# Kernel tuning notes

Measured on AMD Instinct MI355X. Metric: run time of the kernel, lower is better.

Reference implementation:

```python
import jax, jax.numpy as jnp
import numpy as np

B, N, M, H = 32, 1024, 256, 128


def setup_inputs() -> dict:
    key = jax.random.key(0)
    kA, kh, kW1, kW2 = jax.random.split(key, 4)
    A = jax.random.uniform(kA, (B, N, N), dtype=jnp.float32)
    h = jax.random.normal(kh, (B, N, M), dtype=jnp.float32)
    # torch Linear default init scale ~ 1/sqrt(fan_in)
    W1 = jax.random.normal(kW1, (M, H), dtype=jnp.float32) / np.sqrt(M)
    b1 = jnp.zeros((H,), dtype=jnp.float32)
    W2 = jax.random.normal(kW2, (H, M), dtype=jnp.float32) / np.sqrt(H)
    b2 = jnp.zeros((M,), dtype=jnp.float32)
    return {"A": A, "h": h, "W1": W1, "b1": b1, "W2": W2, "b2": b2}


def reference(A, h, W1, b1, W2, b2):
    # k = bmm(A, h) / 3 : [B,N,M]
    k = jnp.einsum('bij,bjm->bim', A, h) / 3.0
    # eta_g: Linear -> ReLU -> Linear
    k = jax.nn.relu(k @ W1 + b1) @ W2 + b2
    # A_mask = max over last dim of A, keepdims -> [B,N,1]
    A_mask = jnp.max(A, axis=-1, keepdims=True)
    # gated combine: k*mask + h*(mask-1)*(-1) == k*mask + h*(1-mask)
    return k * A_mask + h * (1.0 - A_mask)
```

## Files before the change

kernel.cpp:

```cpp
#include <hip/hip_runtime.h>

typedef __attribute__((ext_vector_type(8))) short bf16x8;
typedef __attribute__((ext_vector_type(4))) float f32x4;
typedef __attribute__((ext_vector_type(8))) unsigned short u16x8;

#define BB 32
#define NN 1024
#define MM 256
#define HH 128

__device__ __forceinline__ unsigned short f2bf(float f) {
  union { float f; unsigned int u; } c; c.f = f;
  unsigned int u = c.u + 0x7fffu + ((c.u >> 16) & 1u);
  return (unsigned short)(u >> 16);
}
__device__ __forceinline__ unsigned int cvtpk(float lo, float hi) {
  unsigned int r;
  asm("v_cvt_pk_bf16_f32 %0, %1, %2" : "=v"(r) : "v"(lo), "v"(hi));
  return r;
}
__device__ __forceinline__ float4 gload_f4(const float* p) {
  float4 r;
  asm volatile("global_load_dwordx4 %0, %1, off" : "=v"(r) : "v"(p));
  return r;
}
typedef __attribute__((address_space(3))) unsigned int as3_u32;
typedef const __attribute__((address_space(1))) unsigned int as1_u32;
__device__ __forceinline__ void gl_lds16(const void* g, void* l) {
  __builtin_amdgcn_global_load_lds((as1_u32*)g, (as3_u32*)l, 16, 0, 0);
}

__global__ __launch_bounds__(256)
void k_prep(const float* __restrict__ hg, unsigned short* __restrict__ hTg,
            const float* __restrict__ W1, const float* __restrict__ W2,
            unsigned short* __restrict__ W1T, unsigned short* __restrict__ W2T) {
  int bid = blockIdx.x;
  if (bid < BB * 64) {
    __shared__ unsigned short tile[64][65];
    int b = bid >> 6;
    int t = bid & 63;
    int k0 = (t >> 2) << 6;
    int m0 = (t & 3) << 6;
    int tt = threadIdx.x;
    {
      int r = tt >> 2;
      int cg = (tt & 3) << 4;
      const float* src = hg + (((size_t)b * NN + k0 + r) * MM + m0 + cg);
#pragma unroll
      for (int i = 0; i < 4; ++i) {
        float4 v = reinterpret_cast<const float4*>(src)[i];
        tile[r][cg + i * 4 + 0] = f2bf(v.x);
        tile[r][cg + i * 4 + 1] = f2bf(v.y);
        tile[r][cg + i * 4 + 2] = f2bf(v.z);
        tile[r][cg + i * 4 + 3] = f2bf(v.w);
      }
    }
    __syncthreads();
    {
      int mr = tt >> 2;
      int kc = (tt & 3) << 4;
      alignas(16) unsigned short tmp[16];
#pragma unroll
      for (int i = 0; i < 16; ++i) tmp[i] = tile[kc + i][mr];
      unsigned short* dst = hTg + (((size_t)b * MM + m0 + mr) * NN + k0 + kc);
      *reinterpret_cast<u16x8*>(dst)     = *reinterpret_cast<u16x8*>(tmp);
      *reinterpret_cast<u16x8*>(dst + 8) = *reinterpret_cast<u16x8*>(tmp + 8);
    }
  } else {
    int idx = (bid - BB * 64) * 256 + threadIdx.x;
    if (idx < MM * HH) {
      int hc = idx >> 8;
      int m  = idx & 255;
      W1T[idx] = f2bf(W1[m * HH + hc]);
    } else {
      int j = idx - MM * HH;
      int m  = j >> 7;
      int hd = j & 127;
      W2T[j] = f2bf(W2[hd * MM + m]);
    }
  }
}

#define AB0 0
#define AB1 16384
#define HB0 32768
#define HB1 65536
#define KLD 0
#define CLD 65536

#define PIPE_BARRIER() do { \
  asm volatile("s_waitcnt lgkmcnt(0)" ::: "memory"); \
  __builtin_amdgcn_s_barrier(); \
  asm volatile("" ::: "memory"); } while (0)

#define VMWAIT0() do { \
  asm volatile("s_waitcnt vmcnt(0)" ::: "memory"); \
  __builtin_amdgcn_sched_barrier(0); } while (0)

__global__ __launch_bounds__(512, 1)
void k_fused(const float* __restrict__ Ag, const float* __restrict__ hg,
             const unsigned short* __restrict__ hTg,
             const unsigned short* __restrict__ W1Tg,
             const unsigned short* __restrict__ W2Tg,
             const float* __restrict__ b1g, const float* __restrict__ b2g,
             float* __restrict__ outg) {
  __shared__ __align__(16) char smem[98304];
  __shared__ float smax[128];

  const int tid  = threadIdx.x;
  const int lane = tid & 63;
  const int wid  = tid >> 6;
  const int wr   = wid >> 2;
  const int wc   = wid & 3;
  const int l15  = lane & 15;
  const int lg   = lane >> 4;

  const int bid = blockIdx.x;
  const int b   = bid & 31;
  const int r0  = (bid >> 5) << 7;

  const float* Ab = Ag + ((size_t)b * NN + r0) * NN;
  const unsigned short* hTb = hTg + (size_t)b * MM * NN;

  const int agrp = tid >> 4;
  const int akc  = tid & 15;
  const float* apA0 = Ab + (size_t)(agrp)      * NN + (akc << 2);
  const float* apA1 = Ab + (size_t)(32 + agrp) * NN + (akc << 2);
  const float* apA2 = Ab + (size_t)(64 + agrp) * NN + (akc << 2);
  const float* apA3 = Ab + (size_t)(96 + agrp) * NN + (akc << 2);
  const int asw = (agrp & 7) << 4;

  const unsigned short* baseH[4];
#pragma unroll
  for (int i = 0; i < 4; ++i) {
    int c = i * 512 + tid;
    int col = c >> 3, cic = c & 7;
    baseH[i] = hTb + (size_t)col * NN + ((cic ^ (col & 7)) << 3);
  }
  const int ldsW = wid << 10;

#define STAGE_H(K0, HB)                                                     \
  do {                                                                      \
    _Pragma("unroll")                                                       \
    for (int i = 0; i < 4; ++i)                                             \
      gl_lds16(baseH[i] + (K0), smem + (HB) + ldsW + i * 8192);             \
  } while (0)

  float4 rA0, rA1, rA2, rA3;
#define ISSUE_A(K0)                                                         \
  do {                                                                      \
    rA0 = gload_f4(apA0 + (K0));                                            \
    rA1 = gload_f4(apA1 + (K0));                                            \
    rA2 = gload_f4(apA2 + (K0));                                            \
    rA3 = gload_f4(apA3 + (K0));                                            \
  } while (0)

  float pm0 = -1e30f, pm1 = -1e30f, pm2 = -1e30f, pm3 = -1e30f;
#define CVTWR(AB)                                                           \
  do {                                                                      \
    pm0 = fmaxf(pm0, fmaxf(fmaxf(rA0.x, rA0.y), fmaxf(rA0.z, rA0.w)));      \
    pm1 = fmaxf(pm1, fmaxf(fmaxf(rA1.x, rA1.y), fmaxf(rA1.z, rA1.w)));      \
    pm2 = fmaxf(pm2, fmaxf(fmaxf(rA2.x, rA2.y), fmaxf(rA2.z, rA2.w)));      \
    pm3 = fmaxf(pm3, fmaxf(fmaxf(rA3.x, rA3.y), fmaxf(rA3.z, rA3.w)));      \
    uint2 q0 = make_uint2(cvtpk(rA0.x, rA0.y), cvtpk(rA0.z, rA0.w));        \
    uint2 q1 = make_uint2(cvtpk(rA1.x, rA1.y), cvtpk(rA1.z, rA1.w));        \
    uint2 q2 = make_uint2(cvtpk(rA2.x, rA2.y), cvtpk(rA2.z, rA2.w));        \
    uint2 q3 = make_uint2(cvtpk(rA3.x, rA3.y), cvtpk(rA3.z, rA3.w));        \
    *reinterpret_cast<uint2*>(smem + (AB) + (agrp)      * 128 +             \
                              (((akc << 3)) ^ asw)) = q0;                   \
    *reinterpret_cast<uint2*>(smem + (AB) + (32 + agrp) * 128 +             \
                              (((akc << 3)) ^ asw)) = q1;                   \
    *reinterpret_cast<uint2*>(smem + (AB) + (64 + agrp) * 128 +             \
                              (((akc << 3)) ^ asw)) = q2;                   \
    *reinterpret_cast<uint2*>(smem + (AB) + (96 + agrp) * 128 +             \
                              (((akc << 3)) ^ asw)) = q3;                   \
  } while (0)

  f32x4 acc[4][4];
#pragma unroll
  for (int m = 0; m < 4; ++m)
#pragma unroll
    for (int n = 0; n < 4; ++n) acc[m][n] = f32x4{0.f, 0.f, 0.f, 0.f};

#define CONSUME(AB, HB)                                                     \
  do {                                                                      \
    _Pragma("unroll")                                                       \
    for (int kk = 0; kk < 2; ++kk) {                                        \
      const int kb = (kk * 32 + (lg << 3)) * 2;                             \
      bf16x8 af[4], bh[4];                                                  \
      _Pragma("unroll")                                                     \
      for (int m = 0; m < 4; ++m) {                                         \
        int row = (wr << 6) + (m << 4) + l15;                               \
        af[m] = *reinterpret_cast<const bf16x8*>(                           \
            smem + (AB) + row * 128 + (kb ^ ((row & 7) << 4)));             \
      }                                                                     \
      _Pragma("unroll")                                                     \
      for (int n = 0; n < 4; ++n) {                                         \
        int col = (wc << 6) + (n << 4) + l15;                               \
        bh[n] = *reinterpret_cast<const bf16x8*>(                           \
            smem + (HB) + col * 128 + (kb ^ ((col & 7) << 4)));             \
      }                                                                     \
      _Pragma("unroll")                                                     \
      for (int m = 0; m < 4; ++m)                                           \
        _Pragma("unroll")                                                   \
        for (int n = 0; n < 4; ++n)                                         \
          acc[m][n] = __builtin_amdgcn_mfma_f32_16x16x32_bf16(af[m], bh[n], \
                                                              acc[m][n], 0, 0, 0); \
    }                                                                       \
  } while (0)

  ISSUE_A(0);
  STAGE_H(0, HB0);
  VMWAIT0();
  CVTWR(AB0);
  PIPE_BARRIER();

#pragma unroll
  for (int t = 0; t < 16; ++t) {
    if (t < 15) {
      ISSUE_A((t + 1) * 64);
      STAGE_H((t + 1) * 64, (t & 1) ? HB0 : HB1);
    }
    if (t & 1) CONSUME(AB1, HB1);
    else       CONSUME(AB0, HB0);
    if (t < 15) {
      VMWAIT0();
      if (t & 1) CVTWR(AB0);
      else       CVTWR(AB1);
      PIPE_BARRIER();
    }
  }

  {
    float v0 = pm0, v1 = pm1, v2 = pm2, v3 = pm3;
#pragma unroll
    for (int s = 1; s < 16; s <<= 1) {
      v0 = fmaxf(v0, __shfl_xor(v0, s));
      v1 = fmaxf(v1, __shfl_xor(v1, s));
      v2 = fmaxf(v2, __shfl_xor(v2, s));
      v3 = fmaxf(v3, __shfl_xor(v3, s));
    }
    if ((tid & 15) == 0) {
      smax[agrp]      = v0;
      smax[32 + agrp] = v1;
      smax[64 + agrp] = v2;
      smax[96 + agrp] = v3;
    }
  }
  __syncthreads();

  {
    const float inv3 = 1.0f / 3.0f;
#pragma unroll
    for (int m = 0; m < 4; ++m)
#pragma unroll
      for (int n = 0; n < 4; ++n) {
        int col = (wc << 6) + (n << 4) + l15;
#pragma unroll
        for (int j = 0; j < 4; ++j) {
          int row = (wr << 6) + (m << 4) + (lg << 2) + j;
          *reinterpret_cast<unsigned short*>(smem + KLD + row * 512 +
                                             ((col * 2) ^ ((row & 7) << 4))) =
              f2bf(acc[m][n][j] * inv3);
        }
      }
  }
  __syncthreads();

  f32x4 acc1[4][2];
#pragma unroll
  for (int m = 0; m < 4; ++m)
#pragma unroll
    for (int n = 0; n < 2; ++n) acc1[m][n] = f32x4{0.f, 0.f, 0.f, 0.f};
  const int wcol1 = wc << 5;
#pragma unroll
  for (int kq = 0; kq < 8; ++kq) {
    bf16x8 af[4], bw[2];
#pragma unroll
    for (int m = 0; m < 4; ++m) {
      int row = (wr << 6) + (m << 4) + l15;
      af[m] = *reinterpret_cast<const bf16x8*>(smem + KLD + row * 512 +
              (((kq * 32 + (lg << 3)) * 2) ^ ((row & 7) << 4)));
    }
#pragma unroll
    for (int n = 0; n < 2; ++n) {
      int col = wcol1 + (n << 4) + l15;
      bw[n] = *reinterpret_cast<const bf16x8*>(W1Tg + (size_t)col * 256 +
                                               kq * 32 + (lg << 3));
    }
#pragma unroll
    for (int m = 0; m < 4; ++m)
#pragma unroll
      for (int n = 0; n < 2; ++n)
        acc1[m][n] = __builtin_amdgcn_mfma_f32_16x16x32_bf16(af[m], bw[n], acc1[m][n], 0, 0, 0);
  }

  {
#pragma unroll
    for (int n = 0; n < 2; ++n) {
      int col = wcol1 + (n << 4) + l15;
      float bias = b1g[col];
#pragma unroll
      for (int m = 0; m < 4; ++m)
#pragma unroll
        for (int j = 0; j < 4; ++j) {
          int row = (wr << 6) + (m << 4) + (lg << 2) + j;
          float v = fmaxf(acc1[m][n][j] + bias, 0.f);
          *reinterpret_cast<unsigned short*>(smem + CLD + row * 256 +
                                             ((col * 2) ^ ((row & 7) << 4))) = f2bf(v);
        }
    }
  }
  __syncthreads();

  f32x4 acc2[4][4];
#pragma unroll
  for (int m = 0; m < 4; ++m)
#pragma unroll
    for (int n = 0; n < 4; ++n) acc2[m][n] = f32x4{0.f, 0.f, 0.f, 0.f};
#pragma unroll
  for (int kq = 0; kq < 4; ++kq) {
    bf16x8 af[4], bw[4];
#pragma unroll
    for (int m = 0; m < 4; ++m) {
      int row = (wr << 6) + (m << 4) + l15;
      af[m] = *reinterpret_cast<const bf16x8*>(smem + CLD + row * 256 +
              (((kq * 32 + (lg << 3)) * 2) ^ ((row & 7) << 4)));
    }
#pragma unroll
    for (int n = 0; n < 4; ++n) {
      int col = (wc << 6) + (n << 4) + l15;
      bw[n] = *reinterpret_cast<const bf16x8*>(W2Tg + (size_t)col * 128 +
                                               kq * 32 + (lg << 3));
    }
#pragma unroll
    for (int m = 0; m < 4; ++m)
#pragma unroll
      for (int n = 0; n < 4; ++n)
        acc2[m][n] = __builtin_amdgcn_mfma_f32_16x16x32_bf16(af[m], bw[n], acc2[m][n], 0, 0, 0);
  }

  {
#pragma unroll
    for (int n = 0; n < 4; ++n) {
      int col = (wc << 6) + (n << 4) + l15;
      float b2v = b2g[col];
#pragma unroll
      for (int m = 0; m < 4; ++m)
#pragma unroll
        for (int j = 0; j < 4; ++j) {
          int row = (wr << 6) + (m << 4) + (lg << 2) + j;
          float kv = acc2[m][n][j] + b2v;
          float mask = smax[row];
          size_t gidx = ((size_t)b * NN + r0 + row) * MM + col;
          float hv = hg[gidx];
          outg[gidx] = kv * mask + hv * (1.f - mask);
        }
    }
  }
#undef CONSUME
#undef CVTWR
#undef ISSUE_A
#undef STAGE_H
}

extern "C" void kernel_launch(void* const* d_in, const int* in_sizes, int n_in,
                              void* d_out, int out_size, void* d_ws, size_t ws_size,
                              hipStream_t stream) {
  (void)in_sizes; (void)n_in; (void)out_size; (void)ws_size;
  const float* A  = (const float*)d_in[0];
  const float* h  = (const float*)d_in[1];
  const float* W1 = (const float*)d_in[2];
  const float* b1 = (const float*)d_in[3];
  const float* W2 = (const float*)d_in[4];
  const float* b2 = (const float*)d_in[5];
  float* out = (float*)d_out;

  unsigned short* hT  = (unsigned short*)d_ws;
  unsigned short* W1T = (unsigned short*)((char*)d_ws + (size_t)BB * MM * NN * 2);
  unsigned short* W2T = W1T + MM * HH;

  k_prep<<<BB * 64 + 256, 256, 0, stream>>>(h, hT, W1, W2, W1T, W2T);
  k_fused<<<BB * 8, 512, 0, stream>>>(A, h, hT, W1T, W2T, b1, b2, out);
}
```

Baseline: 63.19 us.

## Halve row tile to 64 and single-buffer A to raise block count

Shrinks each fused block's row tile from 128 to 64 rows, doubling the grid from 256 to 512 blocks so more than one block fits per CU on a 256-CU part. The A staging buffer drops from double to single buffering in LDS, with an extra barrier after each consume, so total LDS falls to about 72KB. The launch-bounds occupancy hint is removed. In exchange, each block re-reads h tiles for half as many rows, which doubles hT traffic, and the added barriers serialize A conversion with compute.

```diff
diff --git a/kernel.cpp b/kernel.cpp
--- a/kernel.cpp
+++ b/kernel.cpp
@@ -81,12 +81,11 @@
   }
 }
 
-#define AB0 0
-#define AB1 16384
-#define HB0 32768
-#define HB1 65536
+#define HB0 0
+#define HB1 32768
+#define ABUF 65536
 #define KLD 0
-#define CLD 65536
+#define CLD 32768
 
 #define PIPE_BARRIER() do { \
   asm volatile("s_waitcnt lgkmcnt(0)" ::: "memory"); \
@@ -97,15 +96,15 @@
   asm volatile("s_waitcnt vmcnt(0)" ::: "memory"); \
   __builtin_amdgcn_sched_barrier(0); } while (0)
 
-__global__ __launch_bounds__(512, 1)
+__global__ __launch_bounds__(512)
 void k_fused(const float* __restrict__ Ag, const float* __restrict__ hg,
              const unsigned short* __restrict__ hTg,
              const unsigned short* __restrict__ W1Tg,
              const unsigned short* __restrict__ W2Tg,
              const float* __restrict__ b1g, const float* __restrict__ b2g,
              float* __restrict__ outg) {
-  __shared__ __align__(16) char smem[98304];
-  __shared__ float smax[128];
+  __shared__ __align__(16) char smem[73728];
+  __shared__ float smax[64];
 
   const int tid  = threadIdx.x;
   const int lane = tid & 63;
@@ -117,18 +116,15 @@
 
   const int bid = blockIdx.x;
   const int b   = bid & 31;
-  const int r0  = (bid >> 5) << 7;
+  const int r0  = (bid >> 5) << 6;
 
   const float* Ab = Ag + ((size_t)b * NN + r0) * NN;
   const unsigned short* hTb = hTg + (size_t)b * MM * NN;
 
-  const int agrp = tid >> 4;
-  const int akc  = tid & 15;
-  const float* apA0 = Ab + (size_t)(agrp)      * NN + (akc << 2);
-  const float* apA1 = Ab + (size_t)(32 + agrp) * NN + (akc << 2);
-  const float* apA2 = Ab + (size_t)(64 + agrp) * NN + (akc << 2);
-  const float* apA3 = Ab + (size_t)(96 + agrp) * NN + (akc << 2);
-  const int asw = (agrp & 7) << 4;
+  const int arow0 = tid >> 4;
+  const int akc   = tid & 15;
+  const float* apA0 = Ab + (size_t)arow0        * NN + (akc << 2);
+  const float* apA1 = Ab + (size_t)(32 + arow0) * NN + (akc << 2);
 
   const unsigned short* baseH[4];
 #pragma unroll
@@ -146,53 +142,43 @@
       gl_lds16(baseH[i] + (K0), smem + (HB) + ldsW + i * 8192);             \
   } while (0)
 
-  float4 rA0, rA1, rA2, rA3;
+  float4 rA0, rA1;
 #define ISSUE_A(K0)                                                         \
   do {                                                                      \
     rA0 = gload_f4(apA0 + (K0));                                            \
     rA1 = gload_f4(apA1 + (K0));                                            \
-    rA2 = gload_f4(apA2 + (K0));                                            \
-    rA3 = gload_f4(apA3 + (K0));                                            \
   } while (0)
 
-  float pm0 = -1e30f, pm1 = -1e30f, pm2 = -1e30f, pm3 = -1e30f;
-#define CVTWR(AB)                                                           \
+  float pm0 = -1e30f, pm1 = -1e30f;
+#define CVTWR()                                                             \
   do {                                                                      \
     pm0 = fmaxf(pm0, fmaxf(fmaxf(rA0.x, rA0.y), fmaxf(rA0.z, rA0.w)));      \
     pm1 = fmaxf(pm1, fmaxf(fmaxf(rA1.x, rA1.y), fmaxf(rA1.z, rA1.w)));      \
-    pm2 = fmaxf(pm2, fmaxf(fmaxf(rA2.x, rA2.y), fmaxf(rA2.z, rA2.w)));      \
-    pm3 = fmaxf(pm3, fmaxf(fmaxf(rA3.x, rA3.y), fmaxf(rA3.z, rA3.w)));      \
     uint2 q0 = make_uint2(cvtpk(rA0.x, rA0.y), cvtpk(rA0.z, rA0.w));        \
     uint2 q1 = make_uint2(cvtpk(rA1.x, rA1.y), cvtpk(rA1.z, rA1.w));        \
-    uint2 q2 = make_uint2(cvtpk(rA2.x, rA2.y), cvtpk(rA2.z, rA2.w));        \
-    uint2 q3 = make_uint2(cvtpk(rA3.x, rA3.y), cvtpk(rA3.z, rA3.w));        \
-    *reinterpret_cast<uint2*>(smem + (AB) + (agrp)      * 128 +             \
-                              (((akc << 3)) ^ asw)) = q0;                   \
-    *reinterpret_cast<uint2*>(smem + (AB) + (32 + agrp) * 128 +             \
-                              (((akc << 3)) ^ asw)) = q1;                   \
-    *reinterpret_cast<uint2*>(smem + (AB) + (64 + agrp) * 128 +             \
-                              (((akc << 3)) ^ asw)) = q2;                   \
-    *reinterpret_cast<uint2*>(smem + (AB) + (96 + agrp) * 128 +             \
-                              (((akc << 3)) ^ asw)) = q3;                   \
+    *reinterpret_cast<uint2*>(smem + ABUF + (arow0)      * 128 +            \
+                              ((akc << 3) ^ ((arow0 & 7) << 4))) = q0;      \
+    *reinterpret_cast<uint2*>(smem + ABUF + (32 + arow0) * 128 +            \
+                              ((akc << 3) ^ ((arow0 & 7) << 4))) = q1;      \
   } while (0)
 
-  f32x4 acc[4][4];
-#pragma unroll
-  for (int m = 0; m < 4; ++m)
+  f32x4 acc[2][4];
+#pragma unroll
+  for (int m = 0; m < 2; ++m)
 #pragma unroll
     for (int n = 0; n < 4; ++n) acc[m][n] = f32x4{0.f, 0.f, 0.f, 0.f};
 
-#define CONSUME(AB, HB)                                                     \
+#define CONSUME(HB)                                                         \
   do {                                                                      \
     _Pragma("unroll")                                                       \
     for (int kk = 0; kk < 2; ++kk) {                                        \
       const int kb = (kk * 32 + (lg << 3)) * 2;                             \
-      bf16x8 af[4], bh[4];                                                  \
+      bf16x8 af[2], bh[4];                                                  \
       _Pragma("unroll")                                                     \
-      for (int m = 0; m < 4; ++m) {                                         \
-        int row = (wr << 6) + (m << 4) + l15;                               \
+      for (int m = 0; m < 2; ++m) {                                         \
+        int row = (wr << 5) + (m << 4) + l15;                               \
         af[m] = *reinterpret_cast<const bf16x8*>(                           \
-            smem + (AB) + row * 128 + (kb ^ ((row & 7) << 4)));             \
+            smem + ABUF + row * 128 + (kb ^ ((row & 7) << 4)));             \
       }                                                                     \
       _Pragma("unroll")                                                     \
       for (int n = 0; n < 4; ++n) {                                         \
@@ -201,7 +187,7 @@
             smem + (HB) + col * 128 + (kb ^ ((col & 7) << 4)));             \
       }                                                                     \
       _Pragma("unroll")                                                     \
-      for (int m = 0; m < 4; ++m)                                           \
+      for (int m = 0; m < 2; ++m)                                           \
         _Pragma("unroll")                                                   \
         for (int n = 0; n < 4; ++n)                                         \
           acc[m][n] = __builtin_amdgcn_mfma_f32_16x16x32_bf16(af[m], bh[n], \
@@ -209,42 +195,37 @@
     }                                                                       \
   } while (0)
 
+  STAGE_H(0, HB0);
   ISSUE_A(0);
-  STAGE_H(0, HB0);
   VMWAIT0();
-  CVTWR(AB0);
+  CVTWR();
   PIPE_BARRIER();
 
 #pragma unroll
   for (int t = 0; t < 16; ++t) {
     if (t < 15) {
+      STAGE_H((t + 1) * 64, (t & 1) ? HB0 : HB1);
       ISSUE_A((t + 1) * 64);
-      STAGE_H((t + 1) * 64, (t & 1) ? HB0 : HB1);
-    }
-    if (t & 1) CONSUME(AB1, HB1);
-    else       CONSUME(AB0, HB0);
+    }
+    CONSUME((t & 1) ? HB1 : HB0);
+    __builtin_amdgcn_s_barrier();
     if (t < 15) {
       VMWAIT0();
-      if (t & 1) CVTWR(AB0);
-      else       CVTWR(AB1);
+      CVTWR();
       PIPE_BARRIER();
     }
   }
 
   {
-    float v0 = pm0, v1 = pm1, v2 = pm2, v3 = pm3;
+    float v0 = pm0, v1 = pm1;
 #pragma unroll
     for (int s = 1; s < 16; s <<= 1) {
       v0 = fmaxf(v0, __shfl_xor(v0, s));
       v1 = fmaxf(v1, __shfl_xor(v1, s));
-      v2 = fmaxf(v2, __shfl_xor(v2, s));
-      v3 = fmaxf(v3, __shfl_xor(v3, s));
     }
     if ((tid & 15) == 0) {
-      smax[agrp]      = v0;
-      smax[32 + agrp] = v1;
-      smax[64 + agrp] = v2;
-      smax[96 + agrp] = v3;
+      smax[arow0]      = v0;
+      smax[32 + arow0] = v1;
     }
   }
   __syncthreads();
@@ -252,13 +233,13 @@
   {
     const float inv3 = 1.0f / 3.0f;
 #pragma unroll
-    for (int m = 0; m < 4; ++m)
+    for (int m = 0; m < 2; ++m)
 #pragma unroll
       for (int n = 0; n < 4; ++n) {
         int col = (wc << 6) + (n << 4) + l15;
 #pragma unroll
         for (int j = 0; j < 4; ++j) {
-          int row = (wr << 6) + (m << 4) + (lg << 2) + j;
+          int row = (wr << 5) + (m << 4) + (lg << 2) + j;
           *reinterpret_cast<unsigned short*>(smem + KLD + row * 512 +
                                              ((col * 2) ^ ((row & 7) << 4))) =
               f2bf(acc[m][n][j] * inv3);
@@ -267,18 +248,18 @@
   }
   __syncthreads();
 
-  f32x4 acc1[4][2];
-#pragma unroll
-  for (int m = 0; m < 4; ++m)
+  f32x4 acc1[2][2];
+#pragma unroll
+  for (int m = 0; m < 2; ++m)
 #pragma unroll
     for (int n = 0; n < 2; ++n) acc1[m][n] = f32x4{0.f, 0.f, 0.f, 0.f};
   const int wcol1 = wc << 5;
 #pragma unroll
   for (int kq = 0; kq < 8; ++kq) {
-    bf16x8 af[4], bw[2];
-#pragma unroll
-    for (int m = 0; m < 4; ++m) {
-      int row = (wr << 6) + (m << 4) + l15;
+    bf16x8 af[2], bw[2];
+#pragma unroll
+    for (int m = 0; m < 2; ++m) {
+      int row = (wr << 5) + (m << 4) + l15;
       af[m] = *reinterpret_cast<const bf16x8*>(smem + KLD + row * 512 +
               (((kq * 32 + (lg << 3)) * 2) ^ ((row & 7) << 4)));
     }
@@ -289,11 +270,12 @@
                                                kq * 32 + (lg << 3));
     }
 #pragma unroll
-    for (int m = 0; m < 4; ++m)
+    for (int m = 0; m < 2; ++m)
 #pragma unroll
       for (int n = 0; n < 2; ++n)
         acc1[m][n] = __builtin_amdgcn_mfma_f32_16x16x32_bf16(af[m], bw[n], acc1[m][n], 0, 0, 0);
   }
+  __syncthreads();
 
   {
 #pragma unroll
@@ -301,10 +283,10 @@
       int col = wcol1 + (n << 4) + l15;
       float bias = b1g[col];
 #pragma unroll
-      for (int m = 0; m < 4; ++m)
+      for (int m = 0; m < 2; ++m)
 #pragma unroll
         for (int j = 0; j < 4; ++j) {
-          int row = (wr << 6) + (m << 4) + (lg << 2) + j;
+          int row = (wr << 5) + (m << 4) + (lg << 2) + j;
           float v = fmaxf(acc1[m][n][j] + bias, 0.f);
           *reinterpret_cast<unsigned short*>(smem + CLD + row * 256 +
                                              ((col * 2) ^ ((row & 7) << 4))) = f2bf(v);
@@ -313,17 +295,17 @@
   }
   __syncthreads();
 
-  f32x4 acc2[4][4];
-#pragma unroll
-  for (int m = 0; m < 4; ++m)
+  f32x4 acc2[2][4];
+#pragma unroll
+  for (int m = 0; m < 2; ++m)
 #pragma unroll
     for (int n = 0; n < 4; ++n) acc2[m][n] = f32x4{0.f, 0.f, 0.f, 0.f};
 #pragma unroll
   for (int kq = 0; kq < 4; ++kq) {
-    bf16x8 af[4], bw[4];
-#pragma unroll
-    for (int m = 0; m < 4; ++m) {
-      int row = (wr << 6) + (m << 4) + l15;
+    bf16x8 af[2], bw[4];
+#pragma unroll
+    for (int m = 0; m < 2; ++m) {
+      int row = (wr << 5) + (m << 4) + l15;
       af[m] = *reinterpret_cast<const bf16x8*>(smem + CLD + row * 256 +
               (((kq * 32 + (lg << 3)) * 2) ^ ((row & 7) << 4)));
     }
@@ -334,7 +316,7 @@
                                                kq * 32 + (lg << 3));
     }
 #pragma unroll
-    for (int m = 0; m < 4; ++m)
+    for (int m = 0; m < 2; ++m)
 #pragma unroll
       for (int n = 0; n < 4; ++n)
         acc2[m][n] = __builtin_amdgcn_mfma_f32_16x16x32_bf16(af[m], bw[n], acc2[m][n], 0, 0, 0);
@@ -346,10 +328,10 @@
       int col = (wc << 6) + (n << 4) + l15;
       float b2v = b2g[col];
 #pragma unroll
-      for (int m = 0; m < 4; ++m)
+      for (int m = 0; m < 2; ++m)
 #pragma unroll
         for (int j = 0; j < 4; ++j) {
-          int row = (wr << 6) + (m << 4) + (lg << 2) + j;
+          int row = (wr << 5) + (m << 4) + (lg << 2) + j;
           float kv = acc2[m][n][j] + b2v;
           float mask = smax[row];
           size_t gidx = ((size_t)b * NN + r0 + row) * MM + col;
@@ -381,5 +363,5 @@
   unsigned short* W2T = W1T + MM * HH;
 
   k_prep<<<BB * 64 + 256, 256, 0, stream>>>(h, hT, W1, W2, W1T, W2T);
-  k_fused<<<BB * 8, 512, 0, stream>>>(A, h, hT, W1T, W2T, b1, b2, out);
-}
+  k_fused<<<BB * 16, 512, 0, stream>>>(A, h, hT, W1T, W2T, b1, b2, out);
+}
```

Result: faster. 58.29 us (-7.8%).
